# Kernel optimization log

Hardware: AMD Instinct MI355X
Metric: run time of the kernel (lower is better)

Reference implementation:

```python
import jax, jax.numpy as jnp
import numpy as np

B, N, D, L, OUT = 4, 256, 256, 128, 256
GAMMA, ETA = 1e-4, 1.0


def _gcn_layer(x, alpha, adj, w_alpha, w_vi, w_vj, bias_h, w_node):
    # x:(B,N,D) alpha:(B,N,N,K) adj:(B,N,N)
    xi = jnp.einsum('bid,dk->bik', x, w_vi)  # project BEFORE broadcast (same math)
    xj = jnp.einsum('bjd,dk->bjk', x, w_vj)
    # bias_h:(D,K) broadcasts against trailing (N,K) dims (requires D==N, as in torch)
    H = jax.nn.relu(xi[:, :, None, :] + xj[:, None, :, :] + alpha + bias_h)  # (B,N,N,K)
    AH = jnp.einsum('bij,bijd->bid', adj, H)
    new_x = jax.nn.relu(jnp.einsum('bid,dk->bik', AH, w_node))
    new_alpha = jax.nn.relu(jnp.einsum('bijd,dk->bijk', H, w_alpha))
    return new_x, new_alpha


def setup_inputs() -> dict:
    key = jax.random.key(0)
    ks = jax.random.split(key, 20)
    inv = lambda fan: 1.0 / np.sqrt(fan)
    x = jax.random.normal(ks[0], (B, N, D), dtype=jnp.float32)
    rel_features = jax.random.normal(ks[1], (B, N, N, 6), dtype=jnp.float32)
    adj = jax.random.uniform(ks[2], (B, N, N), dtype=jnp.float32)
    box_num = jnp.concatenate(
        [jnp.full((1, 1), N, dtype=jnp.int32),
         jax.random.randint(ks[3], (B - 1, 1), N // 2, N + 1, dtype=jnp.int32)], axis=0)
    d = {
        'x': x, 'rel_features': rel_features, 'adj': adj, 'box_num': box_num,
        'W_alpha_t': jax.random.normal(ks[4], (6, D)) * inv(6),
        'b_alpha': jnp.zeros((D,), jnp.float32),
        'W_proj': jax.random.normal(ks[5], (D, L)) * inv(D),
        'b_proj': jnp.zeros((L,), jnp.float32),
        'learn_w': jax.random.uniform(ks[6], (L,)),
    }
    for li, base in ((0, 7), (1, 12)):
        d[f'l{li}_w_alpha'] = jax.random.normal(ks[base + 0], (D, OUT)) * inv(D)
        d[f'l{li}_w_vi'] = jax.random.normal(ks[base + 1], (D, OUT)) * inv(D)
        d[f'l{li}_w_vj'] = jax.random.normal(ks[base + 2], (D, OUT)) * inv(D)
        d[f'l{li}_bias_h'] = jax.random.uniform(ks[base + 3], (D, OUT))
        d[f'l{li}_w_node'] = jax.random.normal(ks[base + 4], (D, OUT)) * inv(D)
    return d


def reference(x, rel_features, adj, box_num, W_alpha_t, b_alpha, W_proj, b_proj, learn_w,
              l0_w_alpha, l0_w_vi, l0_w_vj, l0_bias_h, l0_w_node,
              l1_w_alpha, l1_w_vi, l1_w_vj, l1_bias_h, l1_w_node):
    alpha = jnp.einsum('bijc,cd->bijd', rel_features, W_alpha_t) + b_alpha  # (B,N,N,D)

    # ---- GraphLearningLayer ----
    x_hat = x @ W_proj + b_proj  # (B,N,L)
    valid = jnp.arange(N)[None, :] < box_num  # (B,N)
    pair = valid[:, None, :] & valid[:, :, None]  # (B,N,N)
    mask = jnp.where(pair, 0.0, -1.0)[..., None]  # (~mask)*-1 in torch
    dist = jnp.abs(x_hat[:, :, None, :] - x_hat[:, None, :, :]) + mask  # (B,N,N,L)
    out = jax.nn.leaky_relu(jnp.einsum('bijd,d->bij', dist, learn_w))
    out = out - jnp.max(out, axis=-1, keepdims=True)
    soft_adj = jnp.exp(out) * adj
    soft_adj = soft_adj / jnp.sum(soft_adj, axis=-1, keepdims=True) + 1e-10

    # graph learning loss (training branch)
    diff = x_hat[:, :, None, :] - x_hat[:, None, :, :]
    pair_norm = jnp.sqrt(jnp.sum(diff * diff, axis=-1) + 1e-12)  # (B,N,N)
    bn = box_num.astype(jnp.float32)[:, 0]
    dist_loss = jnp.sum(jnp.exp(soft_adj + ETA * pair_norm), axis=(1, 2)) / (bn * bn)
    f_norm = jnp.sqrt(jnp.sum(soft_adj * soft_adj, axis=(1, 2)))
    gl_loss = dist_loss + GAMMA * f_norm  # (B,)

    # ---- GCN stack ----
    adj2 = adj * soft_adj
    x1, alpha1 = _gcn_layer(x, alpha, adj2, l0_w_alpha, l0_w_vi, l0_w_vj, l0_bias_h, l0_w_node)
    x2, _ = _gcn_layer(x1, alpha1, adj2, l1_w_alpha, l1_w_vi, l1_w_vj, l1_bias_h, l1_w_node)
    return x2, soft_adj, gl_loss
```

## Files before the change

### kernel.cpp

```cpp
#include <hip/hip_runtime.h>

#define NB 4
#define NN 256
#define ND 256
#define NL 128
#define NK 256
static constexpr float GAMMA_C = 1e-4f;
static constexpr float ETA_C = 1.0f;

typedef unsigned int u32;
typedef __attribute__((ext_vector_type(8))) short bf16x8;
typedef __attribute__((ext_vector_type(4))) float f32x4;

__device__ __forceinline__ u32 rne1(float x) {
    u32 a = __float_as_uint(x);
    return (a + 0x7FFFu + ((a >> 16) & 1u)) >> 16;
}
__device__ __forceinline__ float bf2f(u32 v) { return __uint_as_float(v << 16); }
__device__ __forceinline__ u32 pk2bf(float lo, float hi) { return rne1(lo) | (rne1(hi) << 16); }

struct GJob {
    const float* A; const float* W; const float* bias; const float* addm;
    float* C; int Kd; int Nc; int relu;
};

__device__ __forceinline__ void gemm64_body(
    const float* __restrict__ A, const float* __restrict__ W,
    const float* __restrict__ bias, const float* __restrict__ addm,
    float* __restrict__ C, int Kd, int Nc, int relu_act)
{
    __shared__ __align__(16) float As[16][68];
    __shared__ __align__(16) float Ws[16][64];
    int t = threadIdx.x;
    int r0 = blockIdx.x * 64, c0 = blockIdx.y * 64;
    int ty = t >> 4, tx = t & 15;
    float acc[4][4] = {};
    for (int kc = 0; kc < Kd; kc += 16) {
        __syncthreads();
        #pragma unroll
        for (int q = 0; q < 4; ++q) {
            int f = q * 256 + t;
            int row = f >> 4, kk = f & 15;
            As[kk][row] = A[(r0 + row) * Kd + kc + kk];
        }
        #pragma unroll
        for (int q = 0; q < 4; ++q) {
            int f = q * 256 + t;
            int kk = f >> 6, col = f & 63;
            Ws[kk][col] = W[(kc + kk) * Nc + c0 + col];
        }
        __syncthreads();
        #pragma unroll
        for (int kk = 0; kk < 16; ++kk) {
            float4 av = *(const float4*)&As[kk][ty * 4];
            float4 bv = *(const float4*)&Ws[kk][tx * 4];
            float a[4] = {av.x, av.y, av.z, av.w};
            float b[4] = {bv.x, bv.y, bv.z, bv.w};
            #pragma unroll
            for (int i = 0; i < 4; ++i)
                #pragma unroll
                for (int j = 0; j < 4; ++j)
                    acc[i][j] += a[i] * b[j];
        }
    }
    #pragma unroll
    for (int i = 0; i < 4; ++i) {
        int row = r0 + ty * 4 + i;
        #pragma unroll
        for (int j = 0; j < 4; ++j) {
            int col = c0 + tx * 4 + j;
            float v = acc[i][j];
            if (bias) v += bias[col];
            if (addm) v += addm[(row & 255) * Nc + col];
            if (relu_act) v = fmaxf(v, 0.f);
            C[row * Nc + col] = v;
        }
    }
}

__global__ __launch_bounds__(256) void gemm64(
    const float* __restrict__ A, const float* __restrict__ W,
    const float* __restrict__ bias, const float* __restrict__ addm,
    float* __restrict__ C, int M, int Kd, int Nc, int relu_act)
{
    gemm64_body(A, W, bias, addm, C, Kd, Nc, relu_act);
}

__global__ __launch_bounds__(256) void gemm64_multi(GJob j0, GJob j1, GJob j2)
{
    GJob jb = (blockIdx.z == 0) ? j0 : (blockIdx.z == 1) ? j1 : j2;
    if ((int)blockIdx.y * 64 >= jb.Nc) return;
    gemm64_body(jb.A, jb.W, jb.bias, jb.addm, jb.C, jb.Kd, jb.Nc, jb.relu);
}

__global__ __launch_bounds__(256) void soft_adj_kernel(
    const float* __restrict__ xhat, const float* __restrict__ adj,
    const int* __restrict__ box_num, const float* __restrict__ learn_w,
    float* __restrict__ soft_out, float* __restrict__ adj2,
    float* __restrict__ rowP1, float* __restrict__ rowP2)
{
    __shared__ __align__(16) float xs[NL];
    __shared__ __align__(16) float lw[NL];
    __shared__ float red[256];
    int bi = blockIdx.x;
    int b = bi >> 8, i = bi & 255;
    int j = threadIdx.x;
    if (j < NL) { xs[j] = xhat[bi * NL + j]; lw[j] = learn_w[j]; }
    __syncthreads();
    float sumw = 0.f;
    for (int d = 0; d < NL; ++d) sumw += lw[d];
    float s1 = 0.f, s2 = 0.f;
    const float* xj = &xhat[(b * 256 + j) * NL];
    #pragma unroll 4
    for (int d = 0; d < NL; d += 4) {
        float4 a = *(const float4*)&xs[d];
        float4 bb = *(const float4*)&xj[d];
        float d0 = a.x - bb.x, d1 = a.y - bb.y, d2 = a.z - bb.z, d3 = a.w - bb.w;
        s1 += fabsf(d0) * lw[d] + fabsf(d1) * lw[d + 1] + fabsf(d2) * lw[d + 2] + fabsf(d3) * lw[d + 3];
        s2 += d0 * d0 + d1 * d1 + d2 * d2 + d3 * d3;
    }
    int bn = box_num[b];
    float maskv = (i < bn && j < bn) ? 0.f : -1.f;
    float out = s1 + maskv * sumw;
    out = (out >= 0.f) ? out : 0.01f * out;
    float pn = sqrtf(s2 + 1e-12f);
    red[j] = out; __syncthreads();
    for (int s = 128; s > 0; s >>= 1) { if (j < s) red[j] = fmaxf(red[j], red[j + s]); __syncthreads(); }
    float m = red[0]; __syncthreads();
    float aij = adj[bi * 256 + j];
    float e = expf(out - m) * aij;
    red[j] = e; __syncthreads();
    for (int s = 128; s > 0; s >>= 1) { if (j < s) red[j] += red[j + s]; __syncthreads(); }
    float S = red[0]; __syncthreads();
    float soft = e / S + 1e-10f;
    soft_out[bi * 256 + j] = soft;
    adj2[bi * 256 + j] = aij * soft;
    float p1 = expf(soft + ETA_C * pn);
    float p2 = soft * soft;
    red[j] = p1; __syncthreads();
    for (int s = 128; s > 0; s >>= 1) { if (j < s) red[j] += red[j + s]; __syncthreads(); }
    if (j == 0) rowP1[bi] = red[0];
    __syncthreads();
    red[j] = p2; __syncthreads();
    for (int s = 128; s > 0; s >>= 1) { if (j < s) red[j] += red[j + s]; __syncthreads(); }
    if (j == 0) rowP2[bi] = red[0];
}

__global__ __launch_bounds__(256) void gl_loss_kernel(
    const float* __restrict__ rowP1, const float* __restrict__ rowP2,
    const int* __restrict__ box_num, float* __restrict__ out)
{
    __shared__ float r1[256], r2[256];
    int b = blockIdx.x, t = threadIdx.x;
    r1[t] = rowP1[b * 256 + t];
    r2[t] = rowP2[b * 256 + t];
    __syncthreads();
    for (int s = 128; s > 0; s >>= 1) { if (t < s) { r1[t] += r1[t + s]; r2[t] += r2[t + s]; } __syncthreads(); }
    if (t == 0) {
        float bn = (float)box_num[b];
        out[b] = r1[0] / (bn * bn) + GAMMA_C * sqrtf(r2[0]);
    }
}

__global__ __launch_bounds__(256) void wprep(
    const float* __restrict__ w_alpha0, u32* __restrict__ wTp)
{
    int c = blockIdx.x >> 2, kgl = blockIdx.x & 3;
    int n = threadIdx.x;
    #pragma unroll
    for (int q = 0; q < 4; ++q) {
        int k = c * 32 + kgl * 8 + 2 * q;
        float w0 = w_alpha0[k * 256 + n];
        float w1 = w_alpha0[(k + 1) * 256 + n];
        u32 h0 = rne1(w0), h1 = rne1(w1);
        float l0 = w0 - bf2f(h0), l1 = w1 - bf2f(h1);
        wTp[(((0 * 8 + c) * 4 + kgl) * 256 + n) * 4 + q] = h0 | (h1 << 16);
        wTp[(((1 * 8 + c) * 4 + kgl) * 256 + n) * 4 + q] = rne1(l0) | (rne1(l1) << 16);
    }
}

__global__ __launch_bounds__(256, 3) void pass1M(
    const float* __restrict__ rel, const float* __restrict__ Wat,
    const float* __restrict__ b_alpha, const float* __restrict__ xi0,
    const float* __restrict__ xj0b, const float* __restrict__ adj2,
    const u32* __restrict__ wTp,
    u32* __restrict__ alpha1, float* __restrict__ ahpart)
{
    __shared__ __align__(16) float watb_s[256][8];
    __shared__ __align__(16) u32 hsA[2][2][4][64][4];
    __shared__ __align__(16) float st[16][260];

    int t = threadIdx.x;
    int jt = blockIdx.x, it = blockIdx.y, b = blockIdx.z;
    int i0 = it * 8, j0 = jt * 8;
    int m = t & 63, wv = t >> 6;
    int ii = m >> 3, jj = m & 7;
    int l4 = m >> 4, l16 = m & 15;

    #pragma unroll
    for (int q = 0; q < 8; ++q)
        watb_s[t][q] = (q < 6) ? Wat[q * 256 + t] : (q == 6 ? b_alpha[t] : 0.f);
    float relv2[6];
    #pragma unroll
    for (int c = 0; c < 6; ++c)
        relv2[c] = rel[((b * 256 + i0 + ii) * 256 + j0 + jj) * 6 + c];
    float adjv = adj2[(b * 256 + i0 + ii) * 256 + j0 + jj];
    float* ahbase = &ahpart[(((jt * 4 + b) * 32 + it) * 8 + ii) * 256];
    const float* xirow = &xi0[(b * 256 + i0 + ii) * 256];
    const float* xjrow = &xj0b[(b * 256 + j0 + jj) * 256];

    f32x4 acc[4][4];
    #pragma unroll
    for (int a = 0; a < 4; ++a)
        #pragma unroll
        for (int c = 0; c < 4; ++c)
            acc[a][c] = (f32x4){0.f, 0.f, 0.f, 0.f};

    __syncthreads();

    for (int c = 0; c < 8; ++c) {
        int db = c & 1;
        int kb = c * 32 + wv * 8;
        float xiarr[8], xjarr[8];
        {
            float4 x0 = *(const float4*)&xirow[kb];
            float4 x1 = *(const float4*)&xirow[kb + 4];
            xiarr[0]=x0.x; xiarr[1]=x0.y; xiarr[2]=x0.z; xiarr[3]=x0.w;
            xiarr[4]=x1.x; xiarr[5]=x1.y; xiarr[6]=x1.z; xiarr[7]=x1.w;
            float4 y0 = *(const float4*)&xjrow[kb];
            float4 y1 = *(const float4*)&xjrow[kb + 4];
            xjarr[0]=y0.x; xjarr[1]=y0.y; xjarr[2]=y0.z; xjarr[3]=y0.w;
            xjarr[4]=y1.x; xjarr[5]=y1.y; xjarr[6]=y1.z; xjarr[7]=y1.w;
        }
        float h[8];
        #pragma unroll
        for (int i = 0; i < 8; ++i) {
            int k = kb + i;
            float4 wa = *(const float4*)&watb_s[k][0];
            float4 wc = *(const float4*)&watb_s[k][4];
            float a = relv2[0]*wa.x + relv2[1]*wa.y + relv2[2]*wa.z + relv2[3]*wa.w
                    + relv2[4]*wc.x + relv2[5]*wc.y + wc.z;
            h[i] = fmaxf(xiarr[i] + xjarr[i] + a, 0.f);
        }
        {
            float ahv = 0.f;
            #pragma unroll
            for (int i = 0; i < 8; ++i) {
                float v = adjv * h[i];
                v += __shfl_xor(v, 1);
                v += __shfl_xor(v, 2);
                v += __shfl_xor(v, 4);
                ahv = (jj == i) ? v : ahv;
            }
            ahbase[kb + jj] = ahv;
        }
        {
            u32 hi[4], lo[4];
            #pragma unroll
            for (int p = 0; p < 4; ++p) {
                float h0 = h[2*p], h1 = h[2*p+1];
                u32 a0 = rne1(h0), a1 = rne1(h1);
                hi[p] = a0 | (a1 << 16);
                lo[p] = rne1(h0 - bf2f(a0)) | (rne1(h1 - bf2f(a1)) << 16);
            }
            *(uint4*)&hsA[db][0][wv][m][0] = make_uint4(hi[0], hi[1], hi[2], hi[3]);
            *(uint4*)&hsA[db][1][wv][m][0] = make_uint4(lo[0], lo[1], lo[2], lo[3]);
        }
        __syncthreads();

        bf16x8 aH[4], aL[4];
        #pragma unroll
        for (int mt = 0; mt < 4; ++mt) {
            aH[mt] = *(const bf16x8*)&hsA[db][0][l4][mt * 16 + l16][0];
            aL[mt] = *(const bf16x8*)&hsA[db][1][l4][mt * 16 + l16][0];
        }
        const u32* wc0 = &wTp[(c * 4 + l4) * 1024];
        const u32* wc1 = &wTp[((8 + c) * 4 + l4) * 1024];
        #pragma unroll
        for (int ntl = 0; ntl < 4; ++ntl) {
            int n = (wv * 4 + ntl) * 16 + l16;
            bf16x8 bH = *(const bf16x8*)&wc0[n * 4];
            bf16x8 bL = *(const bf16x8*)&wc1[n * 4];
            #pragma unroll
            for (int mt = 0; mt < 4; ++mt) {
                acc[mt][ntl] = __builtin_amdgcn_mfma_f32_16x16x32_bf16(aH[mt], bH, acc[mt][ntl], 0, 0, 0);
                acc[mt][ntl] = __builtin_amdgcn_mfma_f32_16x16x32_bf16(aH[mt], bL, acc[mt][ntl], 0, 0, 0);
                acc[mt][ntl] = __builtin_amdgcn_mfma_f32_16x16x32_bf16(aL[mt], bH, acc[mt][ntl], 0, 0, 0);
            }
        }
        __syncthreads();
    }

    #pragma unroll
    for (int mt = 0; mt < 4; ++mt) {
        #pragma unroll
        for (int ntl = 0; ntl < 4; ++ntl) {
            int n = (wv * 4 + ntl) * 16 + l16;
            #pragma unroll
            for (int r = 0; r < 4; ++r)
                st[l4 * 4 + r][n] = acc[mt][ntl][r];
        }
        __syncthreads();
        #pragma unroll
        for (int p = 0; p < 2; ++p) {
            int f = p * 256 + t;
            int row = f >> 5, u8 = f & 31;
            float4 c0 = *(const float4*)&st[row][u8 * 8];
            float4 c1 = *(const float4*)&st[row][u8 * 8 + 4];
            uint4 pk;
            pk.x = pk2bf(fmaxf(c0.x, 0.f), fmaxf(c0.y, 0.f));
            pk.y = pk2bf(fmaxf(c0.z, 0.f), fmaxf(c0.w, 0.f));
            pk.z = pk2bf(fmaxf(c1.x, 0.f), fmaxf(c1.y, 0.f));
            pk.w = pk2bf(fmaxf(c1.z, 0.f), fmaxf(c1.w, 0.f));
            int mg = mt * 16 + row;
            int iw = mg >> 3, jw = mg & 7;
            *(uint4*)&alpha1[((b * 256 + i0 + iw) * 256 + j0 + jw) * 128 + u8 * 4] = pk;
        }
        __syncthreads();
    }
}

__global__ __launch_bounds__(256) void reduce_ah(
    const float* __restrict__ part, float* __restrict__ AH0)
{
    int bi = blockIdx.x;
    int b = bi >> 8, i = bi & 255;
    int it = i >> 3, ii = i & 7;
    int t = threadIdx.x;
    float s = 0.f;
    for (int jt = 0; jt < 32; ++jt)
        s += part[(((jt * 4 + b) * 32 + it) * 8 + ii) * 256 + t];
    AH0[bi * 256 + t] = s;
}

__global__ __launch_bounds__(256) void pass2b(
    const u32* __restrict__ alpha1, const float* __restrict__ xi1,
    const float* __restrict__ xj1b, const float* __restrict__ adj2,
    float* __restrict__ AH1)
{
    __shared__ __align__(16) float partial[4][256];
    int bi = blockIdx.x;
    int b = bi >> 8;
    int t = threadIdx.x;
    int wv = t >> 6, lane = t & 63;
    int k4 = lane * 4;
    float4 xi = *(const float4*)&xi1[bi * 256 + k4];
    float4 acc = {0.f, 0.f, 0.f, 0.f};
    size_t base = (size_t)bi * 32768;
    const float* a2row = &adj2[bi * 256];
    for (int j = wv; j < 256; j += 4) {
        float a2 = a2row[j];
        float4 xj = *(const float4*)&xj1b[(b * 256 + j) * 256 + k4];
        uint2 q = *(const uint2*)&alpha1[base + j * 128 + (k4 >> 1)];
        float4 al;
        al.x = bf2f(q.x & 0xFFFFu); al.y = bf2f(q.x >> 16);
        al.z = bf2f(q.y & 0xFFFFu); al.w = bf2f(q.y >> 16);
        acc.x += a2 * fmaxf(xi.x + xj.x + al.x, 0.f);
        acc.y += a2 * fmaxf(xi.y + xj.y + al.y, 0.f);
        acc.z += a2 * fmaxf(xi.z + xj.z + al.z, 0.f);
        acc.w += a2 * fmaxf(xi.w + xj.w + al.w, 0.f);
    }
    *(float4*)&partial[wv][k4] = acc;
    __syncthreads();
    if (wv == 0) {
        float4 p0 = *(const float4*)&partial[0][k4];
        float4 p1 = *(const float4*)&partial[1][k4];
        float4 p2 = *(const float4*)&partial[2][k4];
        float4 p3 = *(const float4*)&partial[3][k4];
        float4 o;
        o.x = p0.x + p1.x + p2.x + p3.x;
        o.y = p0.y + p1.y + p2.y + p3.y;
        o.z = p0.z + p1.z + p2.z + p3.z;
        o.w = p0.w + p1.w + p2.w + p3.w;
        *(float4*)&AH1[bi * 256 + k4] = o;
    }
}

__global__ __launch_bounds__(256) void pass1C(
    const float* __restrict__ rel, const float* __restrict__ Wat,
    const float* __restrict__ b_alpha, const float* __restrict__ xi0,
    const float* __restrict__ xj0b, const float* __restrict__ adj2,
    float* __restrict__ AH0)
{
    __shared__ float xj_s[16][257];
    __shared__ float rel_s[16 * 48];
    __shared__ float adj_sC[128];
    int t = threadIdx.x;
    int it = blockIdx.x, b = blockIdx.y;
    int i0 = it * 8;
    float xiv[8], watv[6];
    #pragma unroll
    for (int ii = 0; ii < 8; ++ii) xiv[ii] = xi0[(b * 256 + i0 + ii) * 256 + t];
    #pragma unroll
    for (int c = 0; c < 6; ++c) watv[c] = Wat[c * 256 + t];
    float bav = b_alpha[t];
    float ah[8] = {};
    for (int jc = 0; jc < 256; jc += 16) {
        __syncthreads();
        #pragma unroll
        for (int q = 0; q < 16; ++q) xj_s[q][t] = xj0b[(b * 256 + jc + q) * 256 + t];
        for (int e = t; e < 768; e += 256) {
            int jjp = e / 48, r = e % 48;
            rel_s[e] = rel[((b * 256 + i0 + r / 6) * 256 + jc + jjp) * 6 + (r % 6)];
        }
        if (t < 128) adj_sC[t] = adj2[(b * 256 + i0 + (t & 7)) * 256 + jc + (t >> 3)];
        __syncthreads();
        for (int jjp = 0; jjp < 16; ++jjp) {
            float xjv = xj_s[jjp][t];
            #pragma unroll
            for (int ii = 0; ii < 8; ++ii) {
                float a = bav;
                #pragma unroll
                for (int c = 0; c < 6; ++c) a += rel_s[jjp * 48 + ii * 6 + c] * watv[c];
                float h = fmaxf(xiv[ii] + xjv + a, 0.f);
                ah[ii] += adj_sC[jjp * 8 + ii] * h;
            }
        }
    }
    #pragma unroll
    for (int ii = 0; ii < 8; ++ii)
        AH0[(b * 256 + i0 + ii) * 256 + t] = ah[ii];
}

__global__ __launch_bounds__(256) void pass2C(
    const float* __restrict__ rel, const float* __restrict__ Wat,
    const float* __restrict__ b_alpha, const float* __restrict__ xi0,
    const float* __restrict__ xj0b, const float* __restrict__ w_alpha0,
    const float* __restrict__ xi1, const float* __restrict__ xj1b,
    const float* __restrict__ adj2, float* __restrict__ AH1)
{
    __shared__ float xi_s[8][257];
    __shared__ float xj_s[8][257];
    __shared__ float xj1_s[8][257];
    __shared__ __align__(16) float wat_s[6][256];
    __shared__ __align__(16) float ba_s[256];
    __shared__ __align__(16) float rel_s[6][64];
    __shared__ __align__(16) float adj_s[64];
    __shared__ __align__(16) float hs[16][64];
    __shared__ __align__(16) float ws_s[16][256];

    int t = threadIdx.x;
    int it = blockIdx.x, b = blockIdx.y;
    int i0 = it * 8;
    int rg = t >> 5, cg = t & 31;
    int lane = t & 63, wv = t >> 6;
    int ii_l = lane >> 3, jj_l = lane & 7;

    #pragma unroll
    for (int q = 0; q < 8; ++q) xi_s[q][t] = xi0[(b * 256 + i0 + q) * 256 + t];
    #pragma unroll
    for (int q = 0; q < 6; ++q) wat_s[q][t] = Wat[q * 256 + t];
    ba_s[t] = b_alpha[t];
    float xi1v[8];
    #pragma unroll
    for (int y = 0; y < 8; ++y) xi1v[y] = xi1[(b * 256 + i0 + rg) * 256 + cg * 8 + y];
    float ah1[8] = {};

    for (int jt = 0; jt < 32; ++jt) {
        int j0 = jt * 8;
        __syncthreads();
        #pragma unroll
        for (int q = 0; q < 8; ++q) {
            xj_s[q][t]  = xj0b[(b * 256 + j0 + q) * 256 + t];
            xj1_s[q][t] = xj1b[(b * 256 + j0 + q) * 256 + t];
        }
        for (int e = t; e < 384; e += 256) {
            int ii = e / 48, rem = e % 48;
            int jjp = rem / 6, c = rem % 6;
            rel_s[c][ii * 8 + jjp] = rel[((b * 256 + i0 + ii) * 256 + j0 + jjp) * 6 + c];
        }
        if (t < 64) adj_s[t] = adj2[(b * 256 + i0 + (t >> 3)) * 256 + j0 + (t & 7)];

        float acc[8][8] = {};
        for (int c = 0; c < 16; ++c) {
            __syncthreads();
            #pragma unroll
            for (int p = 0; p < 4; ++p) {
                int klocal = wv + p * 4;
                int kg = c * 16 + klocal;
                float a = ba_s[kg];
                #pragma unroll
                for (int cc = 0; cc < 6; ++cc) a += rel_s[cc][lane] * wat_s[cc][kg];
                float h = xi_s[ii_l][kg] + xj_s[jj_l][kg] + a;
                hs[klocal][lane] = fmaxf(h, 0.f);
            }
            #pragma unroll
            for (int q = 0; q < 4; ++q) {
                int f = q * 256 + t;
                int row = f >> 6, col4 = f & 63;
                *(float4*)&ws_s[row][col4 * 4] =
                    *(const float4*)&w_alpha0[(c * 16 + row) * 256 + col4 * 4];
            }
            __syncthreads();
            #pragma unroll
            for (int kk = 0; kk < 16; ++kk) {
                float4 a0 = *(const float4*)&hs[kk][rg * 8];
                float4 a1 = *(const float4*)&hs[kk][rg * 8 + 4];
                float4 b0 = *(const float4*)&ws_s[kk][cg * 8];
                float4 b1 = *(const float4*)&ws_s[kk][cg * 8 + 4];
                float av[8] = {a0.x, a0.y, a0.z, a0.w, a1.x, a1.y, a1.z, a1.w};
                float bv[8] = {b0.x, b0.y, b0.z, b0.w, b1.x, b1.y, b1.z, b1.w};
                #pragma unroll
                for (int x = 0; x < 8; ++x)
                    #pragma unroll
                    for (int y = 0; y < 8; ++y)
                        acc[x][y] += av[x] * bv[y];
            }
        }
        #pragma unroll
        for (int x = 0; x < 8; ++x) {
            float a2 = adj_s[rg * 8 + x];
            #pragma unroll
            for (int y = 0; y < 8; ++y) {
                float al = fmaxf(acc[x][y], 0.f);
                float h1 = fmaxf(xi1v[y] + xj1_s[x][cg * 8 + y] + al, 0.f);
                ah1[y] += a2 * h1;
            }
        }
    }
    #pragma unroll
    for (int y = 0; y < 8; ++y)
        AH1[(b * 256 + i0 + rg) * 256 + cg * 8 + y] = ah1[y];
}

extern "C" void kernel_launch(void* const* d_in, const int* in_sizes, int n_in,
                              void* d_out, int out_size, void* d_ws, size_t ws_size,
                              hipStream_t stream)
{
    const float* x        = (const float*)d_in[0];
    const float* rel      = (const float*)d_in[1];
    const float* adj      = (const float*)d_in[2];
    const int*   box_num  = (const int*)d_in[3];
    const float* Wat      = (const float*)d_in[4];
    const float* b_alpha  = (const float*)d_in[5];
    const float* W_proj   = (const float*)d_in[6];
    const float* b_proj   = (const float*)d_in[7];
    const float* learn_w  = (const float*)d_in[8];
    const float* w_alpha0 = (const float*)d_in[9];
    const float* w_vi0    = (const float*)d_in[10];
    const float* w_vj0    = (const float*)d_in[11];
    const float* bias_h0  = (const float*)d_in[12];
    const float* w_node0  = (const float*)d_in[13];
    const float* w_vi1    = (const float*)d_in[15];
    const float* w_vj1    = (const float*)d_in[16];
    const float* bias_h1  = (const float*)d_in[17];
    const float* w_node1  = (const float*)d_in[18];

    float* sm    = (float*)d_ws;
    float* adj2  = sm;
    float* xhat  = adj2  + 262144;
    float* xi0   = xhat  + 131072;
    float* xj0b  = xi0   + 262144;
    float* AH0   = xj0b  + 262144;
    float* x1    = AH0   + 262144;
    float* xi1   = x1    + 262144;
    float* xj1b  = xi1   + 262144;
    float* AH1   = xj1b  + 262144;
    float* rowP1 = AH1   + 262144;
    float* rowP2 = rowP1 + 1024;
    const size_t SMALLS_F = 2230272;
    const size_t WTP_F    = 65536;
    const size_t PART_F   = 8388608;
    u32*   wTp    = (u32*)(sm + SMALLS_F);
    float* part   = sm + SMALLS_F + WTP_F;
    u32*   alpha1 = (u32*)(sm + SMALLS_F + WTP_F + PART_F);

    const size_t needM = (SMALLS_F + WTP_F + PART_F) * 4ULL + 134217728ULL;
    int use_mfma = (ws_size >= needM);

    float* out_x2   = (float*)d_out;
    float* out_soft = out_x2 + 262144;
    float* out_gl   = out_soft + 262144;

    if (use_mfma) wprep<<<32, 256, 0, stream>>>(w_alpha0, wTp);

    {
        GJob ja{x, W_proj, b_proj, nullptr, xhat, 256, 128, 0};
        GJob jb{x, w_vi0,  nullptr, nullptr, xi0,  256, 256, 0};
        GJob jc{x, w_vj0,  nullptr, bias_h0, xj0b, 256, 256, 0};
        gemm64_multi<<<dim3(16, 4, 3), 256, 0, stream>>>(ja, jb, jc);
    }
    soft_adj_kernel<<<1024, 256, 0, stream>>>(xhat, adj, box_num, learn_w, out_soft, adj2, rowP1, rowP2);
    gl_loss_kernel<<<4, 256, 0, stream>>>(rowP1, rowP2, box_num, out_gl);

    if (use_mfma) {
        pass1M<<<dim3(32, 32, 4), 256, 0, stream>>>(rel, Wat, b_alpha, xi0, xj0b, adj2, wTp, alpha1, part);
        reduce_ah<<<1024, 256, 0, stream>>>(part, AH0);
    } else {
        pass1C<<<dim3(32, 4), 256, 0, stream>>>(rel, Wat, b_alpha, xi0, xj0b, adj2, AH0);
    }

    gemm64<<<dim3(16, 4), 256, 0, stream>>>(AH0, w_node0, nullptr, nullptr, x1, 1024, 256, 256, 1);
    {
        GJob j1a{x1, w_vi1, nullptr, nullptr, xi1,  256, 256, 0};
        GJob j1b{x1, w_vj1, nullptr, bias_h1, xj1b, 256, 256, 0};
        gemm64_multi<<<dim3(16, 4, 2), 256, 0, stream>>>(j1a, j1b, j1b);
    }

    if (use_mfma) {
        pass2b<<<1024, 256, 0, stream>>>(alpha1, xi1, xj1b, adj2, AH1);
    } else {
        pass2C<<<dim3(32, 4), 256, 0, stream>>>(rel, Wat, b_alpha, xi0, xj0b, w_alpha0, xi1, xj1b, adj2, AH1);
    }

    gemm64<<<dim3(16, 4), 256, 0, stream>>>(AH1, w_node1, nullptr, nullptr, out_x2, 1024, 256, 256, 1);
}
```

Before: 358.9 us.

## Fuse AH reduction with node and projection GEMMs into per-row kernels

In the MFMA path, the AH0 reduction is merged with the layer-0 node GEMM and the layer-1 vi/vj projections into one per-row kernel, post0. The layer-1 node GEMM is folded into the pass2 aggregation kernel, which drops three GEMM launches and the intermediate AH0, x1 and AH1 round trips. Each block now computes its row-vector by matrix products with plain FMAs, so every block re-reads the full weight matrices (256x256 fp32) from cache instead of using tiled GEMMs. bf16 packing also switches to the HIP intrinsic __float22bfloat162_rn, which may map to a hardware convert.

```diff
diff --git a/kernel.cpp b/kernel.cpp
--- a/kernel.cpp
+++ b/kernel.cpp
@@ -1,4 +1,5 @@
 #include <hip/hip_runtime.h>
+#include <hip/hip_bf16.h>
 
 #define NB 4
 #define NN 256
@@ -17,7 +18,11 @@
     return (a + 0x7FFFu + ((a >> 16) & 1u)) >> 16;
 }
 __device__ __forceinline__ float bf2f(u32 v) { return __uint_as_float(v << 16); }
-__device__ __forceinline__ u32 pk2bf(float lo, float hi) { return rne1(lo) | (rne1(hi) << 16); }
+__device__ __forceinline__ u32 pk2(float lo, float hi) {
+    union { __hip_bfloat162 h; u32 u; } cv;
+    cv.h = __float22bfloat162_rn(make_float2(lo, hi));
+    return cv.u;
+}
 
 struct GJob {
     const float* A; const float* W; const float* bias; const float* addm;
@@ -259,9 +264,11 @@
             #pragma unroll
             for (int p = 0; p < 4; ++p) {
                 float h0 = h[2*p], h1 = h[2*p+1];
-                u32 a0 = rne1(h0), a1 = rne1(h1);
-                hi[p] = a0 | (a1 << 16);
-                lo[p] = rne1(h0 - bf2f(a0)) | (rne1(h1 - bf2f(a1)) << 16);
+                u32 hp = pk2(h0, h1);
+                float b0 = __uint_as_float(hp << 16);
+                float b1 = __uint_as_float(hp & 0xFFFF0000u);
+                hi[p] = hp;
+                lo[p] = pk2(h0 - b0, h1 - b1);
             }
             *(uint4*)&hsA[db][0][wv][m][0] = make_uint4(hi[0], hi[1], hi[2], hi[3]);
             *(uint4*)&hsA[db][1][wv][m][0] = make_uint4(lo[0], lo[1], lo[2], lo[3]);
@@ -308,10 +315,10 @@
             float4 c0 = *(const float4*)&st[row][u8 * 8];
             float4 c1 = *(const float4*)&st[row][u8 * 8 + 4];
             uint4 pk;
-            pk.x = pk2bf(fmaxf(c0.x, 0.f), fmaxf(c0.y, 0.f));
-            pk.y = pk2bf(fmaxf(c0.z, 0.f), fmaxf(c0.w, 0.f));
-            pk.z = pk2bf(fmaxf(c1.x, 0.f), fmaxf(c1.y, 0.f));
-            pk.w = pk2bf(fmaxf(c1.z, 0.f), fmaxf(c1.w, 0.f));
+            pk.x = pk2(fmaxf(c0.x, 0.f), fmaxf(c0.y, 0.f));
+            pk.y = pk2(fmaxf(c0.z, 0.f), fmaxf(c0.w, 0.f));
+            pk.z = pk2(fmaxf(c1.x, 0.f), fmaxf(c1.y, 0.f));
+            pk.w = pk2(fmaxf(c1.z, 0.f), fmaxf(c1.w, 0.f));
             int mg = mt * 16 + row;
             int iw = mg >> 3, jw = mg & 7;
             *(uint4*)&alpha1[((b * 256 + i0 + iw) * 256 + j0 + jw) * 128 + u8 * 4] = pk;
@@ -320,25 +327,48 @@
     }
 }
 
-__global__ __launch_bounds__(256) void reduce_ah(
-    const float* __restrict__ part, float* __restrict__ AH0)
-{
+__global__ __launch_bounds__(256) void post0(
+    const float* __restrict__ part, const float* __restrict__ w_node0,
+    const float* __restrict__ w_vi1, const float* __restrict__ w_vj1,
+    const float* __restrict__ bias_h1,
+    float* __restrict__ xi1, float* __restrict__ xj1b)
+{
+    __shared__ __align__(16) float ah_s[256];
+    __shared__ __align__(16) float x1_s[256];
     int bi = blockIdx.x;
     int b = bi >> 8, i = bi & 255;
     int it = i >> 3, ii = i & 7;
     int t = threadIdx.x;
     float s = 0.f;
+    #pragma unroll 4
     for (int jt = 0; jt < 32; ++jt)
         s += part[(((jt * 4 + b) * 32 + it) * 8 + ii) * 256 + t];
-    AH0[bi * 256 + t] = s;
-}
-
-__global__ __launch_bounds__(256) void pass2b(
+    ah_s[t] = s;
+    __syncthreads();
+    float a0 = 0.f;
+    #pragma unroll 8
+    for (int k = 0; k < 256; ++k)
+        a0 += ah_s[k] * w_node0[k * 256 + t];
+    x1_s[t] = fmaxf(a0, 0.f);
+    __syncthreads();
+    float a1 = 0.f, a2 = 0.f;
+    #pragma unroll 8
+    for (int k = 0; k < 256; ++k) {
+        float xv = x1_s[k];
+        a1 += xv * w_vi1[k * 256 + t];
+        a2 += xv * w_vj1[k * 256 + t];
+    }
+    xi1[bi * 256 + t] = a1;
+    xj1b[bi * 256 + t] = a2 + bias_h1[i * 256 + t];
+}
+
+__global__ __launch_bounds__(256) void pass2x(
     const u32* __restrict__ alpha1, const float* __restrict__ xi1,
     const float* __restrict__ xj1b, const float* __restrict__ adj2,
-    float* __restrict__ AH1)
+    const float* __restrict__ w_node1, float* __restrict__ x2)
 {
     __shared__ __align__(16) float partial[4][256];
+    __shared__ __align__(16) float ah1_s[256];
     int bi = blockIdx.x;
     int b = bi >> 8;
     int t = threadIdx.x;
@@ -362,18 +392,13 @@
     }
     *(float4*)&partial[wv][k4] = acc;
     __syncthreads();
-    if (wv == 0) {
-        float4 p0 = *(const float4*)&partial[0][k4];
-        float4 p1 = *(const float4*)&partial[1][k4];
-        float4 p2 = *(const float4*)&partial[2][k4];
-        float4 p3 = *(const float4*)&partial[3][k4];
-        float4 o;
-        o.x = p0.x + p1.x + p2.x + p3.x;
-        o.y = p0.y + p1.y + p2.y + p3.y;
-        o.z = p0.z + p1.z + p2.z + p3.z;
-        o.w = p0.w + p1.w + p2.w + p3.w;
-        *(float4*)&AH1[bi * 256 + k4] = o;
-    }
+    ah1_s[t] = partial[0][t] + partial[1][t] + partial[2][t] + partial[3][t];
+    __syncthreads();
+    float a0 = 0.f;
+    #pragma unroll 8
+    for (int k = 0; k < 256; ++k)
+        a0 += ah1_s[k] * w_node1[k * 256 + t];
+    x2[bi * 256 + t] = fmaxf(a0, 0.f);
 }
 
 __global__ __launch_bounds__(256) void pass1C(
@@ -585,23 +610,17 @@
 
     if (use_mfma) {
         pass1M<<<dim3(32, 32, 4), 256, 0, stream>>>(rel, Wat, b_alpha, xi0, xj0b, adj2, wTp, alpha1, part);
-        reduce_ah<<<1024, 256, 0, stream>>>(part, AH0);
+        post0<<<1024, 256, 0, stream>>>(part, w_node0, w_vi1, w_vj1, bias_h1, xi1, xj1b);
+        pass2x<<<1024, 256, 0, stream>>>(alpha1, xi1, xj1b, adj2, w_node1, out_x2);
     } else {
         pass1C<<<dim3(32, 4), 256, 0, stream>>>(rel, Wat, b_alpha, xi0, xj0b, adj2, AH0);
-    }
-
-    gemm64<<<dim3(16, 4), 256, 0, stream>>>(AH0, w_node0, nullptr, nullptr, x1, 1024, 256, 256, 1);
-    {
-        GJob j1a{x1, w_vi1, nullptr, nullptr, xi1,  256, 256, 0};
-        GJob j1b{x1, w_vj1, nullptr, bias_h1, xj1b, 256, 256, 0};
-        gemm64_multi<<<dim3(16, 4, 2), 256, 0, stream>>>(j1a, j1b, j1b);
-    }
-
-    if (use_mfma) {
-        pass2b<<<1024, 256, 0, stream>>>(alpha1, xi1, xj1b, adj2, AH1);
-    } else {
+        gemm64<<<dim3(16, 4), 256, 0, stream>>>(AH0, w_node0, nullptr, nullptr, x1, 1024, 256, 256, 1);
+        {
+            GJob j1a{x1, w_vi1, nullptr, nullptr, xi1,  256, 256, 0};
+            GJob j1b{x1, w_vj1, nullptr, bias_h1, xj1b, 256, 256, 0};
+            gemm64_multi<<<dim3(16, 4, 2), 256, 0, stream>>>(j1a, j1b, j1b);
+        }
         pass2C<<<dim3(32, 4), 256, 0, stream>>>(rel, Wat, b_alpha, xi0, xj0b, w_alpha0, xi1, xj1b, adj2, AH1);
-    }
-
-    gemm64<<<dim3(16, 4), 256, 0, stream>>>(AH1, w_node1, nullptr, nullptr, out_x2, 1024, 256, 256, 1);
-}
+        gemm64<<<dim3(16, 4), 256, 0, stream>>>(AH1, w_node1, nullptr, nullptr, out_x2, 1024, 256, 256, 1);
+    }
+}
```

Result: faster. 342.0 us (-4.7%).
